# Optimization experiments

Measured on AMD Instinct MI355X. Metric: run time of the kernel, lower is better.

Reference implementation:

```python
import jax, jax.numpy as jnp
import numpy as np

D = 512          # sequence_dim
H = 8            # num_heads
DA = 64          # attn_dim per head
DV = 64          # linear_dim per head
NB = 4           # num_blocks
N = 1024         # max_seq_length + max_output_len + 1
B = 4
EPS = 1e-6


def setup_inputs() -> dict:
    key = jax.random.key(0)
    ks = jax.random.split(key, 8)
    sequence = jax.random.normal(ks[0], (B, N, D), dtype=jnp.float32)
    sequence_length = jax.random.randint(ks[1], (B,), 1, 1014)
    pos_embed = jax.random.normal(ks[2], (N, D), dtype=jnp.float32)  # nn.Embedding ~ N(0,1)
    w_uvqk = jax.random.normal(ks[3], (NB, D, 2 * H * DV + 2 * H * DA), dtype=jnp.float32) * 0.02
    w_o = jax.random.normal(ks[4], (NB, H * DV, D), dtype=jnp.float32) * 0.02
    b_o = jnp.zeros((NB, D), dtype=jnp.float32)
    ln1_g = jnp.ones((NB, D), dtype=jnp.float32)
    ln1_b = jnp.zeros((NB, D), dtype=jnp.float32)
    ln2_g = jnp.ones((NB, H * DV), dtype=jnp.float32)
    ln2_b = jnp.zeros((NB, H * DV), dtype=jnp.float32)
    pos_w = jax.random.normal(ks[5], (NB, 2 * N - 1), dtype=jnp.float32) * 0.02
    return {
        'sequence': sequence, 'sequence_length': sequence_length,
        'pos_embed': pos_embed, 'ln1_g': ln1_g, 'ln1_b': ln1_b,
        'w_uvqk': w_uvqk, 'ln2_g': ln2_g, 'ln2_b': ln2_b,
        'w_o': w_o, 'b_o': b_o, 'pos_w': pos_w,
    }


def _layer_norm(x, g, b):
    mu = jnp.mean(x, axis=-1, keepdims=True)
    var = jnp.mean(jnp.square(x - mu), axis=-1, keepdims=True)
    return (x - mu) * jax.lax.rsqrt(var + EPS) * g + b


def reference(sequence, sequence_length, pos_embed, ln1_g, ln1_b, w_uvqk,
              ln2_g, ln2_b, w_o, b_o, pos_w):
    # positional embedding + scale (inference: dropout = identity)
    x = sequence * jnp.asarray(np.sqrt(D), sequence.dtype) + pos_embed[None, :, :]
    # length mask (dense-padded equivalent of the jagged representation)
    mask = (jnp.arange(N)[None, :] < sequence_length[:, None]).astype(sequence.dtype)[..., None]
    x = x * mask
    # invalid_attn_mask = 1 - triu(ones, diag=1): causal incl. diagonal
    causal = jnp.tril(jnp.ones((N, N), sequence.dtype))
    # rel_pos_bias[i, j] = pos_w[j - i + N - 1]
    idx = jnp.arange(N)
    rel = idx[None, :] - idx[:, None] + (N - 1)  # (N, N) in [0, 2N-2]
    for l in range(NB):
        nx = _layer_norm(x, ln1_g[l], ln1_b[l])
        uvqk = jax.nn.silu(nx @ w_uvqk[l])  # (B, N, 2*H*DV + 2*H*DA)
        u, v, q, k = jnp.split(uvqk, [H * DV, 2 * H * DV, 2 * H * DV + H * DA], axis=-1)
        qh = q.reshape(x.shape[0], N, H, DA)
        kh = k.reshape(x.shape[0], N, H, DA)
        vh = v.reshape(x.shape[0], N, H, DV)
        qk = jnp.einsum('bnhd,bmhd->bhnm', qh, kh) + pos_w[l][rel][None, None]
        attn = jax.nn.silu(qk) * (causal / N)  # (B, H, N, N)
        av = jnp.einsum('bhnm,bmhd->bnhd', attn, vh).reshape(x.shape[0], N, H * DV)
        o_in = _layer_norm(av, ln2_g[l], ln2_b[l]) * u
        x = (x + o_in @ w_o[l] + b_o[l]) * mask  # mask = dense<->jagged roundtrip
    # output_embeddings[..., :D] then L2-normalize with clamped norm
    norm = jnp.linalg.norm(x, axis=-1, keepdims=True)
    return x / jnp.clip(norm, 1e-6, None)
```

## Files before the change

kernel.cpp:

```cpp
#include <hip/hip_runtime.h>
#include <math.h>
#include <stdint.h>

#define NN 1024
#define ROWS 4096
#define NBL 4

typedef _Float16 h8 __attribute__((ext_vector_type(8)));
typedef _Float16 h4 __attribute__((ext_vector_type(4)));
typedef float f4 __attribute__((ext_vector_type(4)));

__device__ __forceinline__ float fast_silu(float x) {
    float e = __builtin_amdgcn_exp2f(-1.4426950408889634f * x);
    return x * __builtin_amdgcn_rcpf(1.0f + e);
}

__device__ __forceinline__ void gl16(const void* gp, void* lp) {
    __builtin_amdgcn_global_load_lds(
        (const __attribute__((address_space(1))) uint32_t*)gp,
        (__attribute__((address_space(3))) uint32_t*)lp, 16, 0, 0);
}

__device__ __forceinline__ float wred(float s) {
    #pragma unroll
    for (int off = 1; off < 64; off <<= 1) s += __shfl_xor(s, off);
    return s;
}

__global__ __launch_bounds__(256) void k_transpose16(const float* __restrict__ wuvqk,
                                                     _Float16* __restrict__ wuT,
                                                     const float* __restrict__ wo,
                                                     _Float16* __restrict__ woT) {
    __shared__ _Float16 T[64][66];
    int z = blockIdx.z;
    const float* s; _Float16* d; int N;
    if (z < 4) { N = 2048; s = wuvqk + (size_t)z * 512 * 2048; d = wuT + (size_t)z * 2048 * 512; }
    else {
        if (blockIdx.x >= 8) return;
        N = 512; s = wo + (size_t)(z - 4) * 512 * 512; d = woT + (size_t)(z - 4) * 512 * 512;
    }
    int n0 = blockIdx.x << 6, k0 = blockIdx.y << 6;
    int tx = threadIdx.x & 63, ty = threadIdx.x >> 6;
    #pragma unroll
    for (int q = 0; q < 16; ++q)
        T[(q << 2) + ty][tx] = (_Float16)s[(size_t)(k0 + (q << 2) + ty) * N + n0 + tx];
    __syncthreads();
    #pragma unroll
    for (int q = 0; q < 16; ++q)
        d[(size_t)(n0 + (q << 2) + ty) * 512 + k0 + tx] = T[tx][(q << 2) + ty];
}

template<int MODE>
__global__ __launch_bounds__(256) void k_lnw(const float* __restrict__ X,
                                             const float* __restrict__ X2,
                                             const float* __restrict__ X3,
                                             const float* __restrict__ seq,
                                             const float* __restrict__ pos,
                                             const int* __restrict__ slen,
                                             const float* __restrict__ g,
                                             const float* __restrict__ bt,
                                             _Float16* __restrict__ O,
                                             const _Float16* __restrict__ U,
                                             float* __restrict__ Xw) {
    int tid = threadIdx.x;
    int w = tid >> 6, lane = tid & 63;
    int c = lane << 3;
    #pragma unroll
    for (int rr = 0; rr < 2; ++rr) {
        int row = (blockIdx.x << 3) + (w << 1) + rr;
        float v[8];
        if (MODE == 1) {
            int b = row >> 10, n = row & (NN - 1);
            float m = (n < slen[b]) ? 1.0f : 0.0f;
            const float4* sp = (const float4*)&seq[(size_t)row * 512 + c];
            const float4* pp = (const float4*)&pos[(size_t)n * 512 + c];
            const float SD = 22.627416997969522f;
            float4 s0 = sp[0], s1 = sp[1], p0 = pp[0], p1 = pp[1];
            v[0]=(s0.x*SD+p0.x)*m; v[1]=(s0.y*SD+p0.y)*m; v[2]=(s0.z*SD+p0.z)*m; v[3]=(s0.w*SD+p0.w)*m;
            v[4]=(s1.x*SD+p1.x)*m; v[5]=(s1.y*SD+p1.y)*m; v[6]=(s1.z*SD+p1.z)*m; v[7]=(s1.w*SD+p1.w)*m;
            float4 o0, o1;
            o0.x=v[0]; o0.y=v[1]; o0.z=v[2]; o0.w=v[3];
            o1.x=v[4]; o1.y=v[5]; o1.z=v[6]; o1.w=v[7];
            float4* xp = (float4*)&Xw[(size_t)row * 512 + c];
            xp[0] = o0; xp[1] = o1;
        } else {
            const float4* xp = (const float4*)&X[(size_t)row * 512 + c];
            float4 a = xp[0], b4 = xp[1];
            v[0]=a.x; v[1]=a.y; v[2]=a.z; v[3]=a.w; v[4]=b4.x; v[5]=b4.y; v[6]=b4.z; v[7]=b4.w;
            if (MODE == 2) {
                int nn = row & (NN - 1);
                if (nn >= 384) {
                    const float4* qp = (const float4*)&X2[(size_t)row * 512 + c];
                    float4 t0 = qp[0], t1 = qp[1];
                    v[0]+=t0.x; v[1]+=t0.y; v[2]+=t0.z; v[3]+=t0.w;
                    v[4]+=t1.x; v[5]+=t1.y; v[6]+=t1.z; v[7]+=t1.w;
                }
                if (nn >= 768) {
                    const float4* qp = (const float4*)&X3[(size_t)row * 512 + c];
                    float4 t0 = qp[0], t1 = qp[1];
                    v[0]+=t0.x; v[1]+=t0.y; v[2]+=t0.z; v[3]+=t0.w;
                    v[4]+=t1.x; v[5]+=t1.y; v[6]+=t1.z; v[7]+=t1.w;
                }
            }
        }
        float s = v[0]+v[1]+v[2]+v[3]+v[4]+v[5]+v[6]+v[7];
        s = wred(s);
        float mu = s * (1.0f / 512.0f);
        float ss = 0.0f;
        #pragma unroll
        for (int i = 0; i < 8; ++i) { float d = v[i] - mu; ss += d * d; }
        ss = wred(ss);
        float rs = rsqrtf(ss * (1.0f / 512.0f) + 1e-6f);

        const float4* gp = (const float4*)&g[c];
        const float4* bp = (const float4*)&bt[c];
        float4 g0 = gp[0], g1 = gp[1], b0 = bp[0], b1 = bp[1];
        float gg[8] = {g0.x,g0.y,g0.z,g0.w,g1.x,g1.y,g1.z,g1.w};
        float bb[8] = {b0.x,b0.y,b0.z,b0.w,b1.x,b1.y,b1.z,b1.w};
        float o[8];
        #pragma unroll
        for (int i = 0; i < 8; ++i) o[i] = (v[i] - mu) * rs * gg[i] + bb[i];
        if (MODE == 2) {
            h8 uu = *(const h8*)&U[(size_t)row * 2048 + c];
            #pragma unroll
            for (int i = 0; i < 8; ++i) o[i] *= (float)uu[i];
        }
        h8 oh;
        #pragma unroll
        for (int i = 0; i < 8; ++i) oh[i] = (_Float16)o[i];
        *(h8*)&O[(size_t)row * 512 + c] = oh;
    }
}

__global__ __launch_bounds__(256) void k_normw(float* __restrict__ X) {
    int tid = threadIdx.x;
    int w = tid >> 6, lane = tid & 63;
    int c = lane << 3;
    #pragma unroll
    for (int rr = 0; rr < 2; ++rr) {
        int row = (blockIdx.x << 3) + (w << 1) + rr;
        float4* xp = (float4*)&X[(size_t)row * 512 + c];
        float4 a = xp[0], b4 = xp[1];
        float ss = a.x*a.x + a.y*a.y + a.z*a.z + a.w*a.w +
                   b4.x*b4.x + b4.y*b4.y + b4.z*b4.z + b4.w*b4.w;
        ss = wred(ss);
        float sc = 1.0f / fmaxf(sqrtf(ss), 1e-6f);
        a.x*=sc; a.y*=sc; a.z*=sc; a.w*=sc; b4.x*=sc; b4.y*=sc; b4.z*=sc; b4.w*=sc;
        xp[0] = a; xp[1] = b4;
    }
}

template<int EPI, int BM, int BN, int WAVES, int WGR, int WGC>
__global__ __launch_bounds__(WAVES * 64) void k_gemm(const _Float16* __restrict__ A,
                                                     const _Float16* __restrict__ Bm,
                                                     _Float16* __restrict__ Cu,
                                                     _Float16* __restrict__ vT,
                                                     const float* __restrict__ bo,
                                                     const int* __restrict__ slen,
                                                     float* __restrict__ Xio) {
    constexpr int WR = BM / WGR / 16;
    constexpr int WC = BN / WGC / 16;
    constexpr int QA = BM * 8 / (WAVES * 64);
    constexpr int QB = BN * 8 / (WAVES * 64);
    __shared__ _Float16 smem[2 * 64 * (BM + BN)];
    _Float16* AsB = smem;
    _Float16* BsB = smem + 2 * BM * 64;
    int tid = threadIdx.x;
    int w = tid >> 6, lane = tid & 63;
    int t = lane & 15, gq = lane >> 4;
    int flat = blockIdx.y * gridDim.x + blockIdx.x;
    int cpx = (gridDim.x * gridDim.y) >> 3;
    int f2 = (flat & 7) * cpx + (flat >> 3);
    int bx = f2 % gridDim.x, by = f2 / gridDim.x;
    int row0 = by * BM, col0 = bx * BN;
    int wr = (w / WGC) * (BM / WGR), wc = (w % WGC) * (BN / WGC);

    f4 zero4 = {0.0f, 0.0f, 0.0f, 0.0f};
    f4 acc[WR][WC];
    #pragma unroll
    for (int i = 0; i < WR; ++i)
        #pragma unroll
        for (int j = 0; j < WC; ++j) acc[i][j] = zero4;

    auto stage = [&](int buf, int k0) {
        _Float16* As = AsB + buf * BM * 64;
        _Float16* Bs = BsB + buf * BN * 64;
        #pragma unroll
        for (int q = 0; q < QA; ++q) {
            int s = (q * WAVES + w) * 64 + lane;
            int r = s >> 3, cs = (s & 7) ^ (r & 7);
            gl16(A + (size_t)(row0 + r) * 512 + k0 + (cs << 3),
                 (char*)As + (size_t)(q * WAVES + w) * 1024);
        }
        #pragma unroll
        for (int q = 0; q < QB; ++q) {
            int s = (q * WAVES + w) * 64 + lane;
            int r = s >> 3, cs = (s & 7) ^ (r & 7);
            gl16(Bm + (size_t)(col0 + r) * 512 + k0 + (cs << 3),
                 (char*)Bs + (size_t)(q * WAVES + w) * 1024);
        }
    };

    stage(0, 0);
    int cur = 0;
    for (int k0 = 0; k0 < 512; k0 += 64) {
        __syncthreads();
        if (k0 + 64 < 512) stage(cur ^ 1, k0 + 64);
        const char* As = (const char*)(AsB + cur * BM * 64);
        const char* Bs = (const char*)(BsB + cur * BN * 64);
        h8 af[WR][2], bf[WC][2];
        #pragma unroll
        for (int i = 0; i < WR; ++i) {
            int rl = wr + (i << 4) + t;
            #pragma unroll
            for (int ks = 0; ks < 2; ++ks)
                af[i][ks] = *(const h8*)(As + rl * 128 + (((gq + (ks << 2)) ^ (rl & 7)) << 4));
        }
        #pragma unroll
        for (int j = 0; j < WC; ++j) {
            int nl = wc + (j << 4) + t;
            #pragma unroll
            for (int ks = 0; ks < 2; ++ks)
                bf[j][ks] = *(const h8*)(Bs + nl * 128 + (((gq + (ks << 2)) ^ (nl & 7)) << 4));
        }
        #pragma unroll
        for (int i = 0; i < WR; ++i)
            #pragma unroll
            for (int j = 0; j < WC; ++j) {
                acc[i][j] = __builtin_amdgcn_mfma_f32_16x16x32_f16(af[i][0], bf[j][0], acc[i][j], 0, 0, 0);
                acc[i][j] = __builtin_amdgcn_mfma_f32_16x16x32_f16(af[i][1], bf[j][1], acc[i][j], 0, 0, 0);
            }
        cur ^= 1;
    }

    if (EPI == 0) {
        _Float16* E = smem;
        bool vblk = (col0 >= 512 && col0 < 1024);
        __syncthreads();
        if (vblk) {
            #pragma unroll
            for (int i = 0; i < WR; ++i)
                #pragma unroll
                for (int j = 0; j < WC; ++j) {
                    int cl = wc + (j << 4) + t;
                    int rl = wr + (i << 4) + (gq << 2);
                    h4 pk;
                    #pragma unroll
                    for (int rr = 0; rr < 4; ++rr) pk[rr] = (_Float16)fast_silu(acc[i][j][rr]);
                    *(h4*)&E[cl * 136 + rl] = pk;
                }
        } else {
            #pragma unroll
            for (int i = 0; i < WR; ++i)
                #pragma unroll
                for (int j = 0; j < WC; ++j) {
                    int cl = wc + (j << 4) + t;
                    int rl = wr + (i << 4) + (gq << 2);
                    #pragma unroll
                    for (int rr = 0; rr < 4; ++rr)
                        E[(rl + rr) * 136 + cl] = (_Float16)fast_silu(acc[i][j][rr]);
                }
        }
        __syncthreads();
        constexpr int ITERS = 128 * 16 / (WAVES * 64);
        if (vblk) {
            int b = row0 >> 10;
            int n0l = row0 & 1023;
            #pragma unroll
            for (int it = 0; it < ITERS; ++it) {
                int dl = it * (WAVES * 4) + (tid >> 4);
                int cc = tid & 15;
                h8 vv = *(const h8*)&E[dl * 136 + (cc << 3)];
                int hh = (col0 + dl - 512) >> 6, dd = (col0 + dl - 512) & 63;
                *(h8*)&vT[((size_t)((b << 3) + hh) * 64 + dd) * 1024 + n0l + (cc << 3)] = vv;
            }
        } else {
            #pragma unroll
            for (int it = 0; it < ITERS; ++it) {
                int rl = it * (WAVES * 4) + (tid >> 4);
                int cc = tid & 15;
                h8 vv = *(const h8*)&E[rl * 136 + (cc << 3)];
                *(h8*)&Cu[(size_t)(row0 + rl) * 2048 + col0 + (cc << 3)] = vv;
            }
        }
    } else {
        #pragma unroll
        for (int i = 0; i < WR; ++i) {
            #pragma unroll
            for (int j = 0; j < WC; ++j) {
                int colf = col0 + wc + (j << 4) + t;
                int rowb = row0 + wr + (i << 4) + (gq << 2);
                int b = rowb >> 10;
                #pragma unroll
                for (int rr = 0; rr < 4; ++rr) {
                    int row = rowb + rr;
                    float m = ((row & 1023) < slen[b]) ? 1.0f : 0.0f;
                    size_t ix = (size_t)row * 512 + colf;
                    Xio[ix] = (Xio[ix] + acc[i][j][rr] + bo[colf]) * m;
                }
            }
        }
    }
}

__global__ __launch_bounds__(256) void k_attn(const _Float16* __restrict__ uvqk,
                                              const _Float16* __restrict__ vT,
                                              const float* __restrict__ posw,
                                              float* __restrict__ av0,
                                              float* __restrict__ av1,
                                              float* __restrict__ av2) {
    __shared__ _Float16 Ks[2][64 * 64];
    __shared__ _Float16 Vs[64 * 64];
    __shared__ _Float16 Ps[64 * 72];
    __shared__ float pws[2][128];
    int tid = threadIdx.x;
    int w = tid >> 6, lane = tid & 63;
    int t = lane & 15, gq = lane >> 4;
    int flat = blockIdx.x + 30 * (blockIdx.y + 8 * blockIdx.z);
    int f2 = (flat & 7) * 120 + (flat >> 3);
    int u = f2 % 30, h = (f2 / 30) & 7, b = f2 / 240;

    int nt, mlo, mhi;
    float* avout;
    if (u < 6) { nt = u; mlo = 0; mhi = nt; avout = av0; }
    else if (u < 18) {
        int p = u - 6; nt = 6 + (p >> 1);
        int c0 = (nt + 2) >> 1;
        if (p & 1) { mlo = c0; mhi = nt; avout = av1; }
        else       { mlo = 0;  mhi = c0 - 1; avout = av0; }
    } else {
        int p = u - 18; int third = p / 3; nt = 12 + third; int q3 = p - 3 * third;
        int c = nt + 1, c1 = (c + 2) / 3, c2 = (2 * c + 2) / 3;
        if (q3 == 0)      { mlo = 0;  mhi = c1 - 1; avout = av0; }
        else if (q3 == 1) { mlo = c1; mhi = c2 - 1; avout = av1; }
        else              { mlo = c2; mhi = nt;     avout = av2; }
    }
    int n0 = nt << 6;

    const _Float16* qbase = uvqk + (size_t)b * NN * 2048 + 1024 + h * 64;
    const _Float16* kbase = uvqk + (size_t)b * NN * 2048 + 1536 + h * 64;
    const _Float16* vbase = vT + (size_t)((b << 3) + h) * 64 * 1024;

    #pragma unroll
    for (int q = 0; q < 2; ++q) {
        int s = (((w << 1) + q) << 6) + lane;
        int r = s >> 3, cs = (s & 7) ^ (r & 7);
        gl16(qbase + (size_t)(n0 + r) * 2048 + (cs << 3),
             (char*)&Ks[1][0] + (size_t)(((w << 1) + q) << 6) * 16);
        gl16(kbase + (size_t)((mlo << 6) + r) * 2048 + (cs << 3),
             (char*)&Ks[0][0] + (size_t)(((w << 1) + q) << 6) * 16);
    }
    if (tid < 128) pws[0][tid] = posw[(mlo << 6) - n0 + tid + 960];
    __syncthreads();

    h8 aq[2];
    {
        int rl = (w << 4) + t;
        #pragma unroll
        for (int ks = 0; ks < 2; ++ks)
            aq[ks] = *(const h8*)((const char*)&Ks[1][0] + rl * 128 +
                                  (((gq + (ks << 2)) ^ (rl & 7)) << 4));
    }
    asm volatile("s_waitcnt lgkmcnt(0)" ::: "memory");
    __builtin_amdgcn_sched_barrier(0);
    __syncthreads();

    f4 zero4 = {0.0f, 0.0f, 0.0f, 0.0f};
    f4 avacc[4];
    #pragma unroll
    for (int j = 0; j < 4; ++j) avacc[j] = zero4;

    int cur = 0;
    for (int mt = mlo; mt <= mhi; ++mt) {
        int m0 = mt << 6;
        #pragma unroll
        for (int q = 0; q < 2; ++q) {
            int s = (((w << 1) + q) << 6) + lane;
            int r = s >> 3, cs = (s & 7) ^ (r & 7);
            gl16(vbase + (size_t)r * 1024 + m0 + (cs << 3),
                 (char*)&Vs[0] + (size_t)(((w << 1) + q) << 6) * 16);
        }
        int mt2 = (mt < mhi) ? mt + 1 : mt;
        #pragma unroll
        for (int q = 0; q < 2; ++q) {
            int s = (((w << 1) + q) << 6) + lane;
            int r = s >> 3, cs = (s & 7) ^ (r & 7);
            gl16(kbase + (size_t)((mt2 << 6) + r) * 2048 + (cs << 3),
                 (char*)&Ks[cur ^ 1][0] + (size_t)(((w << 1) + q) << 6) * 16);
        }
        if (tid < 128) pws[cur ^ 1][tid] = posw[(mt2 << 6) - n0 + tid + 960];

        f4 sacc[4];
        __builtin_amdgcn_s_setprio(1);
        #pragma unroll
        for (int i = 0; i < 4; ++i) {
            f4 binit;
            #pragma unroll
            for (int rr = 0; rr < 4; ++rr)
                binit[rr] = pws[cur][63 + (i << 4) + (gq << 2) + rr - ((w << 4) + t)];
            int ml = (i << 4) + t;
            h8 ak0 = *(const h8*)((const char*)&Ks[cur][0] + ml * 128 + (((gq + 0) ^ (ml & 7)) << 4));
            h8 ak1 = *(const h8*)((const char*)&Ks[cur][0] + ml * 128 + (((gq + 4) ^ (ml & 7)) << 4));
            sacc[i] = __builtin_amdgcn_mfma_f32_16x16x32_f16(ak0, aq[0], binit, 0, 0, 0);
            sacc[i] = __builtin_amdgcn_mfma_f32_16x16x32_f16(ak1, aq[1], sacc[i], 0, 0, 0);
        }
        __builtin_amdgcn_s_setprio(0);
        int nabs = n0 + (w << 4) + t;
        #pragma unroll
        for (int i = 0; i < 4; ++i) {
            int mb = m0 + (i << 4) + (gq << 2);
            h4 pk;
            #pragma unroll
            for (int rr = 0; rr < 4; ++rr) {
                float p = (mb + rr <= nabs) ? fast_silu(sacc[i][rr]) : 0.0f;
                pk[rr] = (_Float16)p;
            }
            *(h4*)((char*)Ps + ((w << 4) + t) * 144 + (i << 5) + (gq << 3)) = pk;
        }
        asm volatile("s_waitcnt lgkmcnt(0)" ::: "memory");
        asm volatile("s_waitcnt vmcnt(2)" ::: "memory");
        __builtin_amdgcn_s_barrier();
        __builtin_amdgcn_s_setprio(1);
        #pragma unroll
        for (int ks = 0; ks < 2; ++ks) {
            h8 pa = *(const h8*)((const char*)Ps + ((w << 4) + t) * 144 + (ks << 6) + (gq << 4));
            #pragma unroll
            for (int jt = 0; jt < 4; ++jt) {
                int dl = (jt << 4) + t;
                h8 bv = *(const h8*)((const char*)&Vs[0] + dl * 128 +
                                     (((gq + (ks << 2)) ^ (dl & 7)) << 4));
                avacc[jt] = __builtin_amdgcn_mfma_f32_16x16x32_f16(pa, bv, avacc[jt], 0, 0, 0);
            }
        }
        __builtin_amdgcn_s_setprio(0);
        __syncthreads();
        cur ^= 1;
    }

    #pragma unroll
    for (int jt = 0; jt < 4; ++jt) {
        #pragma unroll
        for (int rr = 0; rr < 4; ++rr) {
            int n = n0 + (w << 4) + (gq << 2) + rr;
            int d = (jt << 4) + t;
            avout[(size_t)(b * NN + n) * 512 + h * 64 + d] = avacc[jt][rr] * (1.0f / 1024.0f);
        }
    }
}

extern "C" void kernel_launch(void* const* d_in, const int* in_sizes, int n_in,
                              void* d_out, int out_size, void* d_ws, size_t ws_size,
                              hipStream_t stream) {
    const float* seq   = (const float*)d_in[0];
    const int*   slen  = (const int*)d_in[1];
    const float* pos   = (const float*)d_in[2];
    const float* ln1g  = (const float*)d_in[3];
    const float* ln1b  = (const float*)d_in[4];
    const float* wuvqk = (const float*)d_in[5];
    const float* ln2g  = (const float*)d_in[6];
    const float* ln2b  = (const float*)d_in[7];
    const float* wo    = (const float*)d_in[8];
    const float* bo    = (const float*)d_in[9];
    const float* posw  = (const float*)d_in[10];

    float* x = (float*)d_out;
    char* W = (char*)d_ws;
    _Float16* nx16   = (_Float16*)(W);
    _Float16* oin16  = (_Float16*)(W + (4u << 20));
    _Float16* uvqk16 = (_Float16*)(W + (8u << 20));
    _Float16* vT16   = (_Float16*)(W + (24u << 20));
    float*    av0    = (float*)   (W + (28u << 20));
    float*    av1    = (float*)   (W + (36u << 20));
    float*    av2    = (float*)   (W + (44u << 20));
    _Float16* wuT16  = (_Float16*)(W + (52u << 20));
    _Float16* woT16  = (_Float16*)(W + (60u << 20));

    k_transpose16<<<dim3(32, 8, 8), 256, 0, stream>>>(wuvqk, wuT16, wo, woT16);
    for (int l = 0; l < NBL; ++l) {
        if (l == 0)
            k_lnw<1><<<512, 256, 0, stream>>>(nullptr, nullptr, nullptr, seq, pos, slen,
                                              ln1g, ln1b, nx16, nullptr, x);
        else
            k_lnw<0><<<512, 256, 0, stream>>>(x, nullptr, nullptr, nullptr, nullptr, nullptr,
                                              ln1g + l * 512, ln1b + l * 512, nx16, nullptr, nullptr);
        k_gemm<0, 128, 128, 8, 2, 4><<<dim3(16, 32), 512, 0, stream>>>(
            nx16, wuT16 + (size_t)l * 2048 * 512, uvqk16, vT16, nullptr, nullptr, nullptr);
        k_attn<<<dim3(30, 8, NBL), 256, 0, stream>>>(uvqk16, vT16, posw + l * (2 * NN - 1),
                                                     av0, av1, av2);
        k_lnw<2><<<512, 256, 0, stream>>>(av0, av1, av2, nullptr, nullptr, nullptr,
                                          ln2g + l * 512, ln2b + l * 512, oin16, uvqk16, nullptr);
        k_gemm<1, 64, 32, 4, 2, 2><<<dim3(16, 64), 256, 0, stream>>>(
            oin16, woT16 + (size_t)l * 512 * 512, nullptr, nullptr, bo + l * 512, slen, x);
    }
    k_normw<<<512, 256, 0, stream>>>(x);
}
```

Before: 208.7 us.

## Fuse LayerNorm1 into UVQK GEMM by folding gamma/beta into weights

Folds the LN1 gamma into the transposed fp16 weight and precomputes beta·W as a bias in a single prep kernel, which also absorbs the initial embedding/mask step. The UVQK GEMM then reads fp32 x directly, computes per-row mean and rstd itself, stages mean-centred fp16 A tiles through registers, and applies rstd and the bias in the epilogue. This drops a separate LN kernel launch and the nx16 round trip on every layer. In exchange, A loading moves from async global-to-LDS copies to register staging, each row tile repeats the statistics pass, and fp16 rounding happens before normalisation rather than after.

```diff
diff --git a/kernel.cpp b/kernel.cpp
--- a/kernel.cpp
+++ b/kernel.cpp
@@ -27,144 +27,91 @@
     return s;
 }
 
-__global__ __launch_bounds__(256) void k_transpose16(const float* __restrict__ wuvqk,
-                                                     _Float16* __restrict__ wuT,
-                                                     const float* __restrict__ wo,
-                                                     _Float16* __restrict__ woT) {
+__global__ __launch_bounds__(256) void k_prep(const float* __restrict__ wuvqk,
+                                              _Float16* __restrict__ wuT,
+                                              const float* __restrict__ wo,
+                                              _Float16* __restrict__ woT,
+                                              const float* __restrict__ ln1g,
+                                              const float* __restrict__ ln1b,
+                                              float* __restrict__ bias1,
+                                              const float* __restrict__ seq,
+                                              const float* __restrict__ pos,
+                                              const int* __restrict__ slen,
+                                              float* __restrict__ x) {
     __shared__ _Float16 T[64][66];
-    int z = blockIdx.z;
-    const float* s; _Float16* d; int N;
-    if (z < 4) { N = 2048; s = wuvqk + (size_t)z * 512 * 2048; d = wuT + (size_t)z * 2048 * 512; }
-    else {
-        if (blockIdx.x >= 8) return;
-        N = 512; s = wo + (size_t)(z - 4) * 512 * 512; d = woT + (size_t)(z - 4) * 512 * 512;
-    }
-    int n0 = blockIdx.x << 6, k0 = blockIdx.y << 6;
-    int tx = threadIdx.x & 63, ty = threadIdx.x >> 6;
-    #pragma unroll
-    for (int q = 0; q < 16; ++q)
-        T[(q << 2) + ty][tx] = (_Float16)s[(size_t)(k0 + (q << 2) + ty) * N + n0 + tx];
-    __syncthreads();
-    #pragma unroll
-    for (int q = 0; q < 16; ++q)
-        d[(size_t)(n0 + (q << 2) + ty) * 512 + k0 + tx] = T[tx][(q << 2) + ty];
-}
-
-template<int MODE>
-__global__ __launch_bounds__(256) void k_lnw(const float* __restrict__ X,
-                                             const float* __restrict__ X2,
-                                             const float* __restrict__ X3,
-                                             const float* __restrict__ seq,
-                                             const float* __restrict__ pos,
-                                             const int* __restrict__ slen,
-                                             const float* __restrict__ g,
-                                             const float* __restrict__ bt,
-                                             _Float16* __restrict__ O,
-                                             const _Float16* __restrict__ U,
-                                             float* __restrict__ Xw) {
-    int tid = threadIdx.x;
-    int w = tid >> 6, lane = tid & 63;
-    int c = lane << 3;
-    #pragma unroll
-    for (int rr = 0; rr < 2; ++rr) {
-        int row = (blockIdx.x << 3) + (w << 1) + rr;
-        float v[8];
-        if (MODE == 1) {
+    int u = blockIdx.x, tid = threadIdx.x;
+    if (u < 1024) {
+        int z = u >> 8, t = u & 255;
+        int n0 = (t & 31) << 6, k0 = (t >> 5) << 6;
+        const float* s = wuvqk + (size_t)z * 512 * 2048;
+        _Float16* d = wuT + (size_t)z * 2048 * 512;
+        const float* g = ln1g + z * 512;
+        int tx = tid & 63, ty = tid >> 6;
+        #pragma unroll
+        for (int q = 0; q < 16; ++q) {
+            int k = k0 + (q << 2) + ty;
+            T[(q << 2) + ty][tx] = (_Float16)(g[k] * s[(size_t)k * 2048 + n0 + tx]);
+        }
+        __syncthreads();
+        #pragma unroll
+        for (int q = 0; q < 16; ++q)
+            d[(size_t)(n0 + (q << 2) + ty) * 512 + k0 + tx] = T[tx][(q << 2) + ty];
+    } else if (u < 1280) {
+        int v = u - 1024;
+        int z = v >> 6, t = v & 63;
+        int n0 = (t & 7) << 6, k0 = (t >> 3) << 6;
+        const float* s = wo + (size_t)z * 512 * 512;
+        _Float16* d = woT + (size_t)z * 512 * 512;
+        int tx = tid & 63, ty = tid >> 6;
+        #pragma unroll
+        for (int q = 0; q < 16; ++q)
+            T[(q << 2) + ty][tx] = (_Float16)s[(size_t)(k0 + (q << 2) + ty) * 512 + n0 + tx];
+        __syncthreads();
+        #pragma unroll
+        for (int q = 0; q < 16; ++q)
+            d[(size_t)(n0 + (q << 2) + ty) * 512 + k0 + tx] = T[tx][(q << 2) + ty];
+    } else if (u < 1312) {
+        int v = u - 1280;
+        int z = v >> 3, jb = v & 7;
+        int j = (jb << 8) + tid;
+        const float* s = wuvqk + (size_t)z * 512 * 2048;
+        const float* b = ln1b + z * 512;
+        float acc = 0.0f;
+        for (int k = 0; k < 512; ++k) acc = fmaf(b[k], s[(size_t)k * 2048 + j], acc);
+        bias1[z * 2048 + j] = acc;
+    } else {
+        int vb = u - 1312;
+        int w = tid >> 6, lane = tid & 63;
+        int c = lane << 3;
+        #pragma unroll
+        for (int rr = 0; rr < 2; ++rr) {
+            int row = (vb << 3) + (w << 1) + rr;
             int b = row >> 10, n = row & (NN - 1);
             float m = (n < slen[b]) ? 1.0f : 0.0f;
             const float4* sp = (const float4*)&seq[(size_t)row * 512 + c];
             const float4* pp = (const float4*)&pos[(size_t)n * 512 + c];
             const float SD = 22.627416997969522f;
             float4 s0 = sp[0], s1 = sp[1], p0 = pp[0], p1 = pp[1];
-            v[0]=(s0.x*SD+p0.x)*m; v[1]=(s0.y*SD+p0.y)*m; v[2]=(s0.z*SD+p0.z)*m; v[3]=(s0.w*SD+p0.w)*m;
-            v[4]=(s1.x*SD+p1.x)*m; v[5]=(s1.y*SD+p1.y)*m; v[6]=(s1.z*SD+p1.z)*m; v[7]=(s1.w*SD+p1.w)*m;
             float4 o0, o1;
-            o0.x=v[0]; o0.y=v[1]; o0.z=v[2]; o0.w=v[3];
-            o1.x=v[4]; o1.y=v[5]; o1.z=v[6]; o1.w=v[7];
-            float4* xp = (float4*)&Xw[(size_t)row * 512 + c];
+            o0.x = (s0.x * SD + p0.x) * m; o0.y = (s0.y * SD + p0.y) * m;
+            o0.z = (s0.z * SD + p0.z) * m; o0.w = (s0.w * SD + p0.w) * m;
+            o1.x = (s1.x * SD + p1.x) * m; o1.y = (s1.y * SD + p1.y) * m;
+            o1.z = (s1.z * SD + p1.z) * m; o1.w = (s1.w * SD + p1.w) * m;
+            float4* xp = (float4*)&x[(size_t)row * 512 + c];
             xp[0] = o0; xp[1] = o1;
-        } else {
-            const float4* xp = (const float4*)&X[(size_t)row * 512 + c];
-            float4 a = xp[0], b4 = xp[1];
-            v[0]=a.x; v[1]=a.y; v[2]=a.z; v[3]=a.w; v[4]=b4.x; v[5]=b4.y; v[6]=b4.z; v[7]=b4.w;
-            if (MODE == 2) {
-                int nn = row & (NN - 1);
-                if (nn >= 384) {
-                    const float4* qp = (const float4*)&X2[(size_t)row * 512 + c];
-                    float4 t0 = qp[0], t1 = qp[1];
-                    v[0]+=t0.x; v[1]+=t0.y; v[2]+=t0.z; v[3]+=t0.w;
-                    v[4]+=t1.x; v[5]+=t1.y; v[6]+=t1.z; v[7]+=t1.w;
-                }
-                if (nn >= 768) {
-                    const float4* qp = (const float4*)&X3[(size_t)row * 512 + c];
-                    float4 t0 = qp[0], t1 = qp[1];
-                    v[0]+=t0.x; v[1]+=t0.y; v[2]+=t0.z; v[3]+=t0.w;
-                    v[4]+=t1.x; v[5]+=t1.y; v[6]+=t1.z; v[7]+=t1.w;
-                }
-            }
-        }
-        float s = v[0]+v[1]+v[2]+v[3]+v[4]+v[5]+v[6]+v[7];
-        s = wred(s);
-        float mu = s * (1.0f / 512.0f);
-        float ss = 0.0f;
-        #pragma unroll
-        for (int i = 0; i < 8; ++i) { float d = v[i] - mu; ss += d * d; }
-        ss = wred(ss);
-        float rs = rsqrtf(ss * (1.0f / 512.0f) + 1e-6f);
-
-        const float4* gp = (const float4*)&g[c];
-        const float4* bp = (const float4*)&bt[c];
-        float4 g0 = gp[0], g1 = gp[1], b0 = bp[0], b1 = bp[1];
-        float gg[8] = {g0.x,g0.y,g0.z,g0.w,g1.x,g1.y,g1.z,g1.w};
-        float bb[8] = {b0.x,b0.y,b0.z,b0.w,b1.x,b1.y,b1.z,b1.w};
-        float o[8];
-        #pragma unroll
-        for (int i = 0; i < 8; ++i) o[i] = (v[i] - mu) * rs * gg[i] + bb[i];
-        if (MODE == 2) {
-            h8 uu = *(const h8*)&U[(size_t)row * 2048 + c];
-            #pragma unroll
-            for (int i = 0; i < 8; ++i) o[i] *= (float)uu[i];
-        }
-        h8 oh;
-        #pragma unroll
-        for (int i = 0; i < 8; ++i) oh[i] = (_Float16)o[i];
-        *(h8*)&O[(size_t)row * 512 + c] = oh;
-    }
-}
-
-__global__ __launch_bounds__(256) void k_normw(float* __restrict__ X) {
-    int tid = threadIdx.x;
-    int w = tid >> 6, lane = tid & 63;
-    int c = lane << 3;
-    #pragma unroll
-    for (int rr = 0; rr < 2; ++rr) {
-        int row = (blockIdx.x << 3) + (w << 1) + rr;
-        float4* xp = (float4*)&X[(size_t)row * 512 + c];
-        float4 a = xp[0], b4 = xp[1];
-        float ss = a.x*a.x + a.y*a.y + a.z*a.z + a.w*a.w +
-                   b4.x*b4.x + b4.y*b4.y + b4.z*b4.z + b4.w*b4.w;
-        ss = wred(ss);
-        float sc = 1.0f / fmaxf(sqrtf(ss), 1e-6f);
-        a.x*=sc; a.y*=sc; a.z*=sc; a.w*=sc; b4.x*=sc; b4.y*=sc; b4.z*=sc; b4.w*=sc;
-        xp[0] = a; xp[1] = b4;
-    }
-}
-
-template<int EPI, int BM, int BN, int WAVES, int WGR, int WGC>
-__global__ __launch_bounds__(WAVES * 64) void k_gemm(const _Float16* __restrict__ A,
-                                                     const _Float16* __restrict__ Bm,
-                                                     _Float16* __restrict__ Cu,
-                                                     _Float16* __restrict__ vT,
-                                                     const float* __restrict__ bo,
-                                                     const int* __restrict__ slen,
-                                                     float* __restrict__ Xio) {
-    constexpr int WR = BM / WGR / 16;
-    constexpr int WC = BN / WGC / 16;
-    constexpr int QA = BM * 8 / (WAVES * 64);
-    constexpr int QB = BN * 8 / (WAVES * 64);
-    __shared__ _Float16 smem[2 * 64 * (BM + BN)];
+        }
+    }
+}
+
+__global__ __launch_bounds__(512) void k_gemm0f(const float* __restrict__ X,
+                                                const _Float16* __restrict__ Bm,
+                                                const float* __restrict__ B1,
+                                                _Float16* __restrict__ Cu,
+                                                _Float16* __restrict__ vT) {
+    __shared__ _Float16 smem[32768];
+    __shared__ float rsS[128];
     _Float16* AsB = smem;
-    _Float16* BsB = smem + 2 * BM * 64;
+    _Float16* BsB = smem + 2 * 128 * 64;
     int tid = threadIdx.x;
     int w = tid >> 6, lane = tid & 63;
     int t = lane & 15, gq = lane >> 4;
@@ -172,133 +119,150 @@
     int cpx = (gridDim.x * gridDim.y) >> 3;
     int f2 = (flat & 7) * cpx + (flat >> 3);
     int bx = f2 % gridDim.x, by = f2 / gridDim.x;
-    int row0 = by * BM, col0 = bx * BN;
-    int wr = (w / WGC) * (BM / WGR), wc = (w % WGC) * (BN / WGC);
+    int row0 = by * 128, col0 = bx * 128;
+    int wr = (w >> 2) << 6, wc = (w & 3) << 5;
+
+    int ar = tid >> 2;
+    int acb = (tid & 3) << 1;
+    float muR = 0.0f;
+    for (int rr = 0; rr < 16; ++rr) {
+        int r = (w << 4) + rr;
+        const float4* xp = (const float4*)&X[(size_t)(row0 + r) * 512 + (lane << 3)];
+        float4 a = xp[0], b4 = xp[1];
+        float s = a.x + a.y + a.z + a.w + b4.x + b4.y + b4.z + b4.w;
+        s = wred(s);
+        float mu = s * (1.0f / 512.0f);
+        float d0 = a.x - mu, d1 = a.y - mu, d2 = a.z - mu, d3 = a.w - mu;
+        float d4 = b4.x - mu, d5 = b4.y - mu, d6 = b4.z - mu, d7 = b4.w - mu;
+        float ss = d0 * d0; ss += d1 * d1; ss += d2 * d2; ss += d3 * d3;
+        ss += d4 * d4; ss += d5 * d5; ss += d6 * d6; ss += d7 * d7;
+        ss = wred(ss);
+        float rs = rsqrtf(ss * (1.0f / 512.0f) + 1e-6f);
+        if (lane == 0) rsS[r] = rs;
+        if (r == ar) muR = mu;
+    }
+    __syncthreads();
 
     f4 zero4 = {0.0f, 0.0f, 0.0f, 0.0f};
-    f4 acc[WR][WC];
-    #pragma unroll
-    for (int i = 0; i < WR; ++i)
-        #pragma unroll
-        for (int j = 0; j < WC; ++j) acc[i][j] = zero4;
-
-    auto stage = [&](int buf, int k0) {
-        _Float16* As = AsB + buf * BM * 64;
-        _Float16* Bs = BsB + buf * BN * 64;
-        #pragma unroll
-        for (int q = 0; q < QA; ++q) {
-            int s = (q * WAVES + w) * 64 + lane;
-            int r = s >> 3, cs = (s & 7) ^ (r & 7);
-            gl16(A + (size_t)(row0 + r) * 512 + k0 + (cs << 3),
-                 (char*)As + (size_t)(q * WAVES + w) * 1024);
-        }
-        #pragma unroll
-        for (int q = 0; q < QB; ++q) {
-            int s = (q * WAVES + w) * 64 + lane;
+    f4 acc[4][2];
+    #pragma unroll
+    for (int i = 0; i < 4; ++i)
+        #pragma unroll
+        for (int j = 0; j < 2; ++j) acc[i][j] = zero4;
+
+    auto stageA = [&](int buf, int k0) {
+        _Float16* As = AsB + buf * (128 * 64);
+        #pragma unroll
+        for (int q = 0; q < 2; ++q) {
+            int c = acb + q;
+            int col = k0 + (c << 3);
+            const float4* xp = (const float4*)&X[(size_t)(row0 + ar) * 512 + col];
+            float4 a = xp[0], b4 = xp[1];
+            h8 oh;
+            oh[0] = (_Float16)(a.x - muR);  oh[1] = (_Float16)(a.y - muR);
+            oh[2] = (_Float16)(a.z - muR);  oh[3] = (_Float16)(a.w - muR);
+            oh[4] = (_Float16)(b4.x - muR); oh[5] = (_Float16)(b4.y - muR);
+            oh[6] = (_Float16)(b4.z - muR); oh[7] = (_Float16)(b4.w - muR);
+            *(h8*)((char*)As + ar * 128 + ((c ^ (ar & 7)) << 4)) = oh;
+        }
+    };
+    auto stageB = [&](int buf, int k0) {
+        _Float16* Bs = BsB + buf * (128 * 64);
+        #pragma unroll
+        for (int q = 0; q < 2; ++q) {
+            int s = ((q << 3) + w) * 64 + lane;
             int r = s >> 3, cs = (s & 7) ^ (r & 7);
             gl16(Bm + (size_t)(col0 + r) * 512 + k0 + (cs << 3),
-                 (char*)Bs + (size_t)(q * WAVES + w) * 1024);
+                 (char*)Bs + (size_t)((q << 3) + w) * 1024);
         }
     };
 
-    stage(0, 0);
+    stageB(0, 0); stageA(0, 0);
     int cur = 0;
     for (int k0 = 0; k0 < 512; k0 += 64) {
         __syncthreads();
-        if (k0 + 64 < 512) stage(cur ^ 1, k0 + 64);
-        const char* As = (const char*)(AsB + cur * BM * 64);
-        const char* Bs = (const char*)(BsB + cur * BN * 64);
-        h8 af[WR][2], bf[WC][2];
-        #pragma unroll
-        for (int i = 0; i < WR; ++i) {
+        if (k0 + 64 < 512) { stageB(cur ^ 1, k0 + 64); stageA(cur ^ 1, k0 + 64); }
+        const char* As = (const char*)(AsB + cur * (128 * 64));
+        const char* Bs = (const char*)(BsB + cur * (128 * 64));
+        h8 af[4][2], bf[2][2];
+        #pragma unroll
+        for (int i = 0; i < 4; ++i) {
             int rl = wr + (i << 4) + t;
             #pragma unroll
             for (int ks = 0; ks < 2; ++ks)
                 af[i][ks] = *(const h8*)(As + rl * 128 + (((gq + (ks << 2)) ^ (rl & 7)) << 4));
         }
         #pragma unroll
-        for (int j = 0; j < WC; ++j) {
+        for (int j = 0; j < 2; ++j) {
             int nl = wc + (j << 4) + t;
             #pragma unroll
             for (int ks = 0; ks < 2; ++ks)
                 bf[j][ks] = *(const h8*)(Bs + nl * 128 + (((gq + (ks << 2)) ^ (nl & 7)) << 4));
         }
         #pragma unroll
-        for (int i = 0; i < WR; ++i)
-            #pragma unroll
-            for (int j = 0; j < WC; ++j) {
+        for (int i = 0; i < 4; ++i)
+            #pragma unroll
+            for (int j = 0; j < 2; ++j) {
                 acc[i][j] = __builtin_amdgcn_mfma_f32_16x16x32_f16(af[i][0], bf[j][0], acc[i][j], 0, 0, 0);
                 acc[i][j] = __builtin_amdgcn_mfma_f32_16x16x32_f16(af[i][1], bf[j][1], acc[i][j], 0, 0, 0);
             }
         cur ^= 1;
     }
 
-    if (EPI == 0) {
-        _Float16* E = smem;
-        bool vblk = (col0 >= 512 && col0 < 1024);
-        __syncthreads();
-        if (vblk) {
-            #pragma unroll
-            for (int i = 0; i < WR; ++i)
+    _Float16* E = smem;
+    bool vblk = (col0 >= 512 && col0 < 1024);
+    __syncthreads();
+    float b1v[2];
+    #pragma unroll
+    for (int j = 0; j < 2; ++j) b1v[j] = B1[col0 + wc + (j << 4) + t];
+    if (vblk) {
+        #pragma unroll
+        for (int i = 0; i < 4; ++i) {
+            int rl = wr + (i << 4) + (gq << 2);
+            f4 rv = *(f4*)&rsS[rl];
+            #pragma unroll
+            for (int j = 0; j < 2; ++j) {
+                int cl = wc + (j << 4) + t;
+                h4 pk;
                 #pragma unroll
-                for (int j = 0; j < WC; ++j) {
-                    int cl = wc + (j << 4) + t;
-                    int rl = wr + (i << 4) + (gq << 2);
-                    h4 pk;
-                    #pragma unroll
-                    for (int rr = 0; rr < 4; ++rr) pk[rr] = (_Float16)fast_silu(acc[i][j][rr]);
-                    *(h4*)&E[cl * 136 + rl] = pk;
-                }
-        } else {
-            #pragma unroll
-            for (int i = 0; i < WR; ++i)
+                for (int rr = 0; rr < 4; ++rr)
+                    pk[rr] = (_Float16)fast_silu(rv[rr] * acc[i][j][rr] + b1v[j]);
+                *(h4*)&E[cl * 136 + rl] = pk;
+            }
+        }
+    } else {
+        #pragma unroll
+        for (int i = 0; i < 4; ++i) {
+            int rl = wr + (i << 4) + (gq << 2);
+            f4 rv = *(f4*)&rsS[rl];
+            #pragma unroll
+            for (int j = 0; j < 2; ++j) {
+                int cl = wc + (j << 4) + t;
                 #pragma unroll
-                for (int j = 0; j < WC; ++j) {
-                    int cl = wc + (j << 4) + t;
-                    int rl = wr + (i << 4) + (gq << 2);
-                    #pragma unroll
-                    for (int rr = 0; rr < 4; ++rr)
-                        E[(rl + rr) * 136 + cl] = (_Float16)fast_silu(acc[i][j][rr]);
-                }
-        }
-        __syncthreads();
-        constexpr int ITERS = 128 * 16 / (WAVES * 64);
-        if (vblk) {
-            int b = row0 >> 10;
-            int n0l = row0 & 1023;
-            #pragma unroll
-            for (int it = 0; it < ITERS; ++it) {
-                int dl = it * (WAVES * 4) + (tid >> 4);
-                int cc = tid & 15;
-                h8 vv = *(const h8*)&E[dl * 136 + (cc << 3)];
-                int hh = (col0 + dl - 512) >> 6, dd = (col0 + dl - 512) & 63;
-                *(h8*)&vT[((size_t)((b << 3) + hh) * 64 + dd) * 1024 + n0l + (cc << 3)] = vv;
+                for (int rr = 0; rr < 4; ++rr)
+                    E[(rl + rr) * 136 + cl] = (_Float16)fast_silu(rv[rr] * acc[i][j][rr] + b1v[j]);
             }
-        } else {
-            #pragma unroll
-            for (int it = 0; it < ITERS; ++it) {
-                int rl = it * (WAVES * 4) + (tid >> 4);
-                int cc = tid & 15;
-                h8 vv = *(const h8*)&E[rl * 136 + (cc << 3)];
-                *(h8*)&Cu[(size_t)(row0 + rl) * 2048 + col0 + (cc << 3)] = vv;
-            }
+        }
+    }
+    __syncthreads();
+    if (vblk) {
+        int b = row0 >> 10;
+        int n0l = row0 & 1023;
+        #pragma unroll
+        for (int it = 0; it < 4; ++it) {
+            int dl = (it << 5) + (tid >> 4);
+            int cc = tid & 15;
+            h8 vv = *(const h8*)&E[dl * 136 + (cc << 3)];
+            int hh = (col0 + dl - 512) >> 6, dd = (col0 + dl - 512) & 63;
+            *(h8*)&vT[((size_t)((b << 3) + hh) * 64 + dd) * 1024 + n0l + (cc << 3)] = vv;
         }
     } else {
         #pragma unroll
-        for (int i = 0; i < WR; ++i) {
-            #pragma unroll
-            for (int j = 0; j < WC; ++j) {
-                int colf = col0 + wc + (j << 4) + t;
-                int rowb = row0 + wr + (i << 4) + (gq << 2);
-                int b = rowb >> 10;
-                #pragma unroll
-                for (int rr = 0; rr < 4; ++rr) {
-                    int row = rowb + rr;
-                    float m = ((row & 1023) < slen[b]) ? 1.0f : 0.0f;
-                    size_t ix = (size_t)row * 512 + colf;
-                    Xio[ix] = (Xio[ix] + acc[i][j][rr] + bo[colf]) * m;
-                }
-            }
+        for (int it = 0; it < 4; ++it) {
+            int rl = (it << 5) + (tid >> 4);
+            int cc = tid & 15;
+            h8 vv = *(const h8*)&E[rl * 136 + (cc << 3)];
+            *(h8*)&Cu[(size_t)(row0 + rl) * 2048 + col0 + (cc << 3)] = vv;
         }
     }
 }
@@ -448,6 +412,161 @@
     }
 }
 
+__global__ __launch_bounds__(256) void k_ln2(const float* __restrict__ X,
+                                             const float* __restrict__ X2,
+                                             const float* __restrict__ X3,
+                                             const float* __restrict__ g,
+                                             const float* __restrict__ bt,
+                                             _Float16* __restrict__ O,
+                                             const _Float16* __restrict__ U) {
+    int tid = threadIdx.x;
+    int w = tid >> 6, lane = tid & 63;
+    int c = lane << 3;
+    #pragma unroll
+    for (int rr = 0; rr < 2; ++rr) {
+        int row = (blockIdx.x << 3) + (w << 1) + rr;
+        const float4* xp = (const float4*)&X[(size_t)row * 512 + c];
+        float4 a = xp[0], b4 = xp[1];
+        float v[8] = {a.x, a.y, a.z, a.w, b4.x, b4.y, b4.z, b4.w};
+        int nn = row & (NN - 1);
+        if (nn >= 384) {
+            const float4* qp = (const float4*)&X2[(size_t)row * 512 + c];
+            float4 t0 = qp[0], t1 = qp[1];
+            v[0]+=t0.x; v[1]+=t0.y; v[2]+=t0.z; v[3]+=t0.w;
+            v[4]+=t1.x; v[5]+=t1.y; v[6]+=t1.z; v[7]+=t1.w;
+        }
+        if (nn >= 768) {
+            const float4* qp = (const float4*)&X3[(size_t)row * 512 + c];
+            float4 t0 = qp[0], t1 = qp[1];
+            v[0]+=t0.x; v[1]+=t0.y; v[2]+=t0.z; v[3]+=t0.w;
+            v[4]+=t1.x; v[5]+=t1.y; v[6]+=t1.z; v[7]+=t1.w;
+        }
+        float s = v[0]+v[1]+v[2]+v[3]+v[4]+v[5]+v[6]+v[7];
+        s = wred(s);
+        float mu = s * (1.0f / 512.0f);
+        float ss = 0.0f;
+        #pragma unroll
+        for (int i = 0; i < 8; ++i) { float d = v[i] - mu; ss += d * d; }
+        ss = wred(ss);
+        float rs = rsqrtf(ss * (1.0f / 512.0f) + 1e-6f);
+
+        const float4* gp = (const float4*)&g[c];
+        const float4* bp = (const float4*)&bt[c];
+        float4 g0 = gp[0], g1 = gp[1], b0 = bp[0], b1 = bp[1];
+        float gg[8] = {g0.x,g0.y,g0.z,g0.w,g1.x,g1.y,g1.z,g1.w};
+        float bb[8] = {b0.x,b0.y,b0.z,b0.w,b1.x,b1.y,b1.z,b1.w};
+        h8 uu = *(const h8*)&U[(size_t)row * 2048 + c];
+        h8 oh;
+        #pragma unroll
+        for (int i = 0; i < 8; ++i)
+            oh[i] = (_Float16)(((v[i] - mu) * rs * gg[i] + bb[i]) * (float)uu[i]);
+        *(h8*)&O[(size_t)row * 512 + c] = oh;
+    }
+}
+
+__global__ __launch_bounds__(256) void k_gemm1(const _Float16* __restrict__ A,
+                                               const _Float16* __restrict__ Bm,
+                                               const float* __restrict__ bo,
+                                               const int* __restrict__ slen,
+                                               float* __restrict__ Xio) {
+    __shared__ _Float16 smem[2 * 64 * 96];
+    _Float16* AsB = smem;
+    _Float16* BsB = smem + 2 * 64 * 64;
+    int tid = threadIdx.x;
+    int w = tid >> 6, lane = tid & 63;
+    int t = lane & 15, gq = lane >> 4;
+    int flat = blockIdx.y * gridDim.x + blockIdx.x;
+    int cpx = (gridDim.x * gridDim.y) >> 3;
+    int f2 = (flat & 7) * cpx + (flat >> 3);
+    int bx = f2 % gridDim.x, by = f2 / gridDim.x;
+    int row0 = by * 64, col0 = bx * 32;
+    int wr = (w >> 1) << 5, wc = (w & 1) << 4;
+
+    f4 zero4 = {0.0f, 0.0f, 0.0f, 0.0f};
+    f4 acc[2];
+    acc[0] = zero4; acc[1] = zero4;
+
+    auto stage = [&](int buf, int k0) {
+        _Float16* As = AsB + buf * (64 * 64);
+        _Float16* Bs = BsB + buf * (32 * 64);
+        #pragma unroll
+        for (int q = 0; q < 2; ++q) {
+            int s = ((q << 2) + w) * 64 + lane;
+            int r = s >> 3, cs = (s & 7) ^ (r & 7);
+            gl16(A + (size_t)(row0 + r) * 512 + k0 + (cs << 3),
+                 (char*)As + (size_t)((q << 2) + w) * 1024);
+        }
+        {
+            int s = (w << 6) + lane;
+            int r = s >> 3, cs = (s & 7) ^ (r & 7);
+            gl16(Bm + (size_t)(col0 + r) * 512 + k0 + (cs << 3),
+                 (char*)Bs + (size_t)w * 1024);
+        }
+    };
+
+    stage(0, 0);
+    int cur = 0;
+    for (int k0 = 0; k0 < 512; k0 += 64) {
+        __syncthreads();
+        if (k0 + 64 < 512) stage(cur ^ 1, k0 + 64);
+        const char* As = (const char*)(AsB + cur * (64 * 64));
+        const char* Bs = (const char*)(BsB + cur * (32 * 64));
+        h8 af[2][2], bf[2];
+        #pragma unroll
+        for (int i = 0; i < 2; ++i) {
+            int rl = wr + (i << 4) + t;
+            #pragma unroll
+            for (int ks = 0; ks < 2; ++ks)
+                af[i][ks] = *(const h8*)(As + rl * 128 + (((gq + (ks << 2)) ^ (rl & 7)) << 4));
+        }
+        {
+            int nl = wc + t;
+            #pragma unroll
+            for (int ks = 0; ks < 2; ++ks)
+                bf[ks] = *(const h8*)(Bs + nl * 128 + (((gq + (ks << 2)) ^ (nl & 7)) << 4));
+        }
+        #pragma unroll
+        for (int i = 0; i < 2; ++i) {
+            acc[i] = __builtin_amdgcn_mfma_f32_16x16x32_f16(af[i][0], bf[0], acc[i], 0, 0, 0);
+            acc[i] = __builtin_amdgcn_mfma_f32_16x16x32_f16(af[i][1], bf[1], acc[i], 0, 0, 0);
+        }
+        cur ^= 1;
+    }
+
+    int colf = col0 + wc + t;
+    float bov = bo[colf];
+    #pragma unroll
+    for (int i = 0; i < 2; ++i) {
+        int rowb = row0 + wr + (i << 4) + (gq << 2);
+        int b = rowb >> 10;
+        #pragma unroll
+        for (int rr = 0; rr < 4; ++rr) {
+            int row = rowb + rr;
+            float m = ((row & 1023) < slen[b]) ? 1.0f : 0.0f;
+            size_t ix = (size_t)row * 512 + colf;
+            Xio[ix] = (Xio[ix] + acc[i][rr] + bov) * m;
+        }
+    }
+}
+
+__global__ __launch_bounds__(256) void k_normw(float* __restrict__ X) {
+    int tid = threadIdx.x;
+    int w = tid >> 6, lane = tid & 63;
+    int c = lane << 3;
+    #pragma unroll
+    for (int rr = 0; rr < 2; ++rr) {
+        int row = (blockIdx.x << 3) + (w << 1) + rr;
+        float4* xp = (float4*)&X[(size_t)row * 512 + c];
+        float4 a = xp[0], b4 = xp[1];
+        float ss = a.x*a.x + a.y*a.y + a.z*a.z + a.w*a.w +
+                   b4.x*b4.x + b4.y*b4.y + b4.z*b4.z + b4.w*b4.w;
+        ss = wred(ss);
+        float sc = 1.0f / fmaxf(sqrtf(ss), 1e-6f);
+        a.x*=sc; a.y*=sc; a.z*=sc; a.w*=sc; b4.x*=sc; b4.y*=sc; b4.z*=sc; b4.w*=sc;
+        xp[0] = a; xp[1] = b4;
+    }
+}
+
 extern "C" void kernel_launch(void* const* d_in, const int* in_sizes, int n_in,
                               void* d_out, int out_size, void* d_ws, size_t ws_size,
                               hipStream_t stream) {
@@ -465,32 +584,27 @@
 
     float* x = (float*)d_out;
     char* W = (char*)d_ws;
-    _Float16* nx16   = (_Float16*)(W);
-    _Float16* oin16  = (_Float16*)(W + (4u << 20));
-    _Float16* uvqk16 = (_Float16*)(W + (8u << 20));
-    _Float16* vT16   = (_Float16*)(W + (24u << 20));
-    float*    av0    = (float*)   (W + (28u << 20));
-    float*    av1    = (float*)   (W + (36u << 20));
-    float*    av2    = (float*)   (W + (44u << 20));
-    _Float16* wuT16  = (_Float16*)(W + (52u << 20));
-    _Float16* woT16  = (_Float16*)(W + (60u << 20));
-
-    k_transpose16<<<dim3(32, 8, 8), 256, 0, stream>>>(wuvqk, wuT16, wo, woT16);
+    _Float16* oin16  = (_Float16*)(W);
+    _Float16* uvqk16 = (_Float16*)(W + (4u << 20));
+    _Float16* vT16   = (_Float16*)(W + (20u << 20));
+    float*    av0    = (float*)   (W + (24u << 20));
+    float*    av1    = (float*)   (W + (32u << 20));
+    float*    av2    = (float*)   (W + (40u << 20));
+    _Float16* wuT16  = (_Float16*)(W + (48u << 20));
+    _Float16* woT16  = (_Float16*)(W + (56u << 20));
+    float*    bias1  = (float*)   (W + (58u << 20));
+
+    k_prep<<<1824, 256, 0, stream>>>(wuvqk, wuT16, wo, woT16, ln1g, ln1b, bias1,
+                                     seq, pos, slen, x);
     for (int l = 0; l < NBL; ++l) {
-        if (l == 0)
-            k_lnw<1><<<512, 256, 0, stream>>>(nullptr, nullptr, nullptr, seq, pos, slen,
-                                              ln1g, ln1b, nx16, nullptr, x);
-        else
-            k_lnw<0><<<512, 256, 0, stream>>>(x, nullptr, nullptr, nullptr, nullptr, nullptr,
-                                              ln1g + l * 512, ln1b + l * 512, nx16, nullptr, nullptr);
-        k_gemm<0, 128, 128, 8, 2, 4><<<dim3(16, 32), 512, 0, stream>>>(
-            nx16, wuT16 + (size_t)l * 2048 * 512, uvqk16, vT16, nullptr, nullptr, nullptr);
+        k_gemm0f<<<dim3(16, 32), 512, 0, stream>>>(
+            x, wuT16 + (size_t)l * 2048 * 512, bias1 + l * 2048, uvqk16, vT16);
         k_attn<<<dim3(30, 8, NBL), 256, 0, stream>>>(uvqk16, vT16, posw + l * (2 * NN - 1),
                                                      av0, av1, av2);
-        k_lnw<2><<<512, 256, 0, stream>>>(av0, av1, av2, nullptr, nullptr, nullptr,
-                                          ln2g + l * 512, ln2b + l * 512, oin16, uvqk16, nullptr);
-        k_gemm<1, 64, 32, 4, 2, 2><<<dim3(16, 64), 256, 0, stream>>>(
-            oin16, woT16 + (size_t)l * 512 * 512, nullptr, nullptr, bo + l * 512, slen, x);
+        k_ln2<<<512, 256, 0, stream>>>(av0, av1, av2, ln2g + l * 512, ln2b + l * 512,
+                                       oin16, uvqk16);
+        k_gemm1<<<dim3(16, 64), 256, 0, stream>>>(oin16, woT16 + (size_t)l * 512 * 512,
+                                                  bo + l * 512, slen, x);
     }
     k_normw<<<512, 256, 0, stream>>>(x);
 }
```

New measurement: 276.1 us. 1.32x slower.

## Pipeline GEMM and attention loads with explicit vmcnt waits and V double-buffering

Applied to the files above, without the earlier changes.

The GEMM main loop now issues the next K-slice prefetch before synchronising. It waits only on the current buffer's loads via vmcnt and uses raw s_barrier calls, in place of a __syncthreads before the prefetch. The attention kernel double-buffers the V tile so V for the next key block is prefetched alongside K. It also loads the whole relative-position bias span into shared memory once, instead of staging 128 values per iteration. The goal is to hide global-to-LDS load latency behind MFMA work and drop one barrier per attention iteration. The cost is more LDS and correctness that depends on hand-counted vmcnt values.

```diff
diff --git a/kernel.cpp b/kernel.cpp
--- a/kernel.cpp
+++ b/kernel.cpp
@@ -162,6 +162,7 @@
     constexpr int WC = BN / WGC / 16;
     constexpr int QA = BM * 8 / (WAVES * 64);
     constexpr int QB = BN * 8 / (WAVES * 64);
+    constexpr int NL = QA + QB;
     __shared__ _Float16 smem[2 * 64 * (BM + BN)];
     _Float16* AsB = smem;
     _Float16* BsB = smem + 2 * BM * 64;
@@ -204,8 +205,14 @@
     stage(0, 0);
     int cur = 0;
     for (int k0 = 0; k0 < 512; k0 += 64) {
-        __syncthreads();
-        if (k0 + 64 < 512) stage(cur ^ 1, k0 + 64);
+        if (k0 + 64 < 512) {
+            stage(cur ^ 1, k0 + 64);
+            asm volatile("s_waitcnt vmcnt(%0)" :: "n"(NL) : "memory");
+        } else {
+            asm volatile("s_waitcnt vmcnt(0)" ::: "memory");
+        }
+        __builtin_amdgcn_s_barrier();
+        __builtin_amdgcn_sched_barrier(0);
         const char* As = (const char*)(AsB + cur * BM * 64);
         const char* Bs = (const char*)(BsB + cur * BN * 64);
         h8 af[WR][2], bf[WC][2];
@@ -230,6 +237,8 @@
                 acc[i][j] = __builtin_amdgcn_mfma_f32_16x16x32_f16(af[i][0], bf[j][0], acc[i][j], 0, 0, 0);
                 acc[i][j] = __builtin_amdgcn_mfma_f32_16x16x32_f16(af[i][1], bf[j][1], acc[i][j], 0, 0, 0);
             }
+        __builtin_amdgcn_s_barrier();
+        __builtin_amdgcn_sched_barrier(0);
         cur ^= 1;
     }
 
@@ -310,9 +319,9 @@
                                               float* __restrict__ av1,
                                               float* __restrict__ av2) {
     __shared__ _Float16 Ks[2][64 * 64];
-    __shared__ _Float16 Vs[64 * 64];
+    __shared__ _Float16 Vs[2][64 * 64];
     __shared__ _Float16 Ps[64 * 72];
-    __shared__ float pws[2][128];
+    __shared__ float pwall[1088];
     int tid = threadIdx.x;
     int w = tid >> 6, lane = tid & 63;
     int t = lane & 15, gq = lane >> 4;
@@ -346,11 +355,17 @@
         int s = (((w << 1) + q) << 6) + lane;
         int r = s >> 3, cs = (s & 7) ^ (r & 7);
         gl16(qbase + (size_t)(n0 + r) * 2048 + (cs << 3),
-             (char*)&Ks[1][0] + (size_t)(((w << 1) + q) << 6) * 16);
+             (char*)&Ks[1][0] + (((w << 1) + q) << 10));
         gl16(kbase + (size_t)((mlo << 6) + r) * 2048 + (cs << 3),
-             (char*)&Ks[0][0] + (size_t)(((w << 1) + q) << 6) * 16);
-    }
-    if (tid < 128) pws[0][tid] = posw[(mlo << 6) - n0 + tid + 960];
+             (char*)&Ks[0][0] + (((w << 1) + q) << 10));
+        gl16(vbase + (size_t)r * 1024 + (mlo << 6) + (cs << 3),
+             (char*)&Vs[0][0] + (((w << 1) + q) << 10));
+    }
+    {
+        int span = ((mhi - mlo) << 6) + 128;
+        int base2 = (mlo << 6) - n0 + 960;
+        for (int idx = tid; idx < span; idx += 256) pwall[idx] = posw[base2 + idx];
+    }
     __syncthreads();
 
     h8 aq[2];
@@ -373,31 +388,28 @@
     int cur = 0;
     for (int mt = mlo; mt <= mhi; ++mt) {
         int m0 = mt << 6;
-        #pragma unroll
-        for (int q = 0; q < 2; ++q) {
-            int s = (((w << 1) + q) << 6) + lane;
-            int r = s >> 3, cs = (s & 7) ^ (r & 7);
-            gl16(vbase + (size_t)r * 1024 + m0 + (cs << 3),
-                 (char*)&Vs[0] + (size_t)(((w << 1) + q) << 6) * 16);
-        }
         int mt2 = (mt < mhi) ? mt + 1 : mt;
         #pragma unroll
         for (int q = 0; q < 2; ++q) {
             int s = (((w << 1) + q) << 6) + lane;
             int r = s >> 3, cs = (s & 7) ^ (r & 7);
             gl16(kbase + (size_t)((mt2 << 6) + r) * 2048 + (cs << 3),
-                 (char*)&Ks[cur ^ 1][0] + (size_t)(((w << 1) + q) << 6) * 16);
-        }
-        if (tid < 128) pws[cur ^ 1][tid] = posw[(mt2 << 6) - n0 + tid + 960];
+                 (char*)&Ks[cur ^ 1][0] + (((w << 1) + q) << 10));
+            gl16(vbase + (size_t)r * 1024 + (mt2 << 6) + (cs << 3),
+                 (char*)&Vs[cur ^ 1][0] + (((w << 1) + q) << 10));
+        }
+        asm volatile("s_waitcnt vmcnt(4)" ::: "memory");
+        __builtin_amdgcn_s_barrier();
+        __builtin_amdgcn_sched_barrier(0);
 
         f4 sacc[4];
         __builtin_amdgcn_s_setprio(1);
         #pragma unroll
         for (int i = 0; i < 4; ++i) {
             f4 binit;
-            #pragma unroll
-            for (int rr = 0; rr < 4; ++rr)
-                binit[rr] = pws[cur][63 + (i << 4) + (gq << 2) + rr - ((w << 4) + t)];
+            int pb = ((mt - mlo) << 6) + 63 + (i << 4) + (gq << 2) - ((w << 4) + t);
+            #pragma unroll
+            for (int rr = 0; rr < 4; ++rr) binit[rr] = pwall[pb + rr];
             int ml = (i << 4) + t;
             h8 ak0 = *(const h8*)((const char*)&Ks[cur][0] + ml * 128 + (((gq + 0) ^ (ml & 7)) << 4));
             h8 ak1 = *(const h8*)((const char*)&Ks[cur][0] + ml * 128 + (((gq + 4) ^ (ml & 7)) << 4));
@@ -418,8 +430,7 @@
             *(h4*)((char*)Ps + ((w << 4) + t) * 144 + (i << 5) + (gq << 3)) = pk;
         }
         asm volatile("s_waitcnt lgkmcnt(0)" ::: "memory");
-        asm volatile("s_waitcnt vmcnt(2)" ::: "memory");
-        __builtin_amdgcn_s_barrier();
+        __builtin_amdgcn_sched_barrier(0);
         __builtin_amdgcn_s_setprio(1);
         #pragma unroll
         for (int ks = 0; ks < 2; ++ks) {
@@ -427,15 +438,17 @@
             #pragma unroll
             for (int jt = 0; jt < 4; ++jt) {
                 int dl = (jt << 4) + t;
-                h8 bv = *(const h8*)((const char*)&Vs[0] + dl * 128 +
+                h8 bv = *(const h8*)((const char*)&Vs[cur][0] + dl * 128 +
                                      (((gq + (ks << 2)) ^ (dl & 7)) << 4));
                 avacc[jt] = __builtin_amdgcn_mfma_f32_16x16x32_f16(pa, bv, avacc[jt], 0, 0, 0);
             }
         }
         __builtin_amdgcn_s_setprio(0);
-        __syncthreads();
+        __builtin_amdgcn_s_barrier();
+        __builtin_amdgcn_sched_barrier(0);
         cur ^= 1;
     }
+    asm volatile("s_waitcnt vmcnt(0)" ::: "memory");
 
     #pragma unroll
     for (int jt = 0; jt < 4; ++jt) {
```

New measurement: 223.8 us. 1.07x slower.
